# Optimization experiments

Measured on AMD Instinct MI355X. Metric: run time of the kernel, lower is better.

## Reference

```python
import jax, jax.numpy as jnp
import numpy as np

C = 64            # in_channels
IC = C // 2       # inter_channels (channel_rate=2)
R = 16            # reduction_ratio
EPS = 1e-5


def setup_inputs() -> dict:
    key = jax.random.key(0)
    ks = jax.random.split(key, 16)
    s = 0.05
    return {
        "x": jax.random.normal(ks[0], (16, C, 64, 25), dtype=jnp.float32),
        # 1x1 conv projections (common_v, key, query): [out, in] + bias
        "Wv": jax.random.normal(ks[1], (IC, C), dtype=jnp.float32) * s,
        "bv": jax.random.normal(ks[2], (IC,), dtype=jnp.float32) * s,
        "Wk": jax.random.normal(ks[3], (IC, C), dtype=jnp.float32) * s,
        "bk": jax.random.normal(ks[4], (IC,), dtype=jnp.float32) * s,
        "Wq": jax.random.normal(ks[5], (IC, C), dtype=jnp.float32) * s,
        "bq": jax.random.normal(ks[6], (IC,), dtype=jnp.float32) * s,
        # Trans_s: conv1x1 back to C + BatchNorm2d params (nonzero so output is non-trivial)
        "Wt": jax.random.normal(ks[7], (C, IC), dtype=jnp.float32) * s,
        "bt": jax.random.normal(ks[8], (C,), dtype=jnp.float32) * s,
        "gamma": jax.random.normal(ks[9], (C,), dtype=jnp.float32) * 0.5 + 1.0,
        "beta": jax.random.normal(ks[10], (C,), dtype=jnp.float32) * s,
        # ChannelGate MLP: Linear(C, C//R), Linear(C//R, C)
        "W1": jax.random.normal(ks[11], (C // R, C), dtype=jnp.float32) * s,
        "b1": jax.random.normal(ks[12], (C // R,), dtype=jnp.float32) * s,
        "W2": jax.random.normal(ks[13], (C, C // R), dtype=jnp.float32) * s,
        "b2": jax.random.normal(ks[14], (C,), dtype=jnp.float32) * s,
    }


def _conv1x1(x, W, b):
    # x: [N, Cin, T, V]; W: [Cout, Cin]
    return jnp.einsum('nctv,oc->notv', x, W) + b[None, :, None, None]


def reference(x, Wv, bv, Wk, bk, Wq, bq, Wt, bt, gamma, beta, W1, b1, W2, b2):
    N, Cc, T, V = x.shape
    TV = T * V
    ic = Wv.shape[0]

    v_x = _conv1x1(x, Wv, bv).reshape(N, ic, TV).transpose(0, 2, 1)  # [N, TV, ic]
    k_x = _conv1x1(x, Wk, bk).reshape(N, ic, TV).transpose(0, 2, 1)  # [N, TV, ic]
    q_x = _conv1x1(x, Wq, bq).reshape(N, ic, TV)                      # [N, ic, TV]

    # Unscaled dot-product attention over TV tokens (full [N, TV, TV] matrix)
    A = jnp.einsum('nti,nis->nts', k_x, q_x)
    attn = jax.nn.softmax(A, axis=-1)
    p = jnp.einsum('nts,nsi->nti', attn, v_x)                         # [N, TV, ic]
    p = p.transpose(0, 2, 1).reshape(N, ic, T, V)

    # Trans_s: conv1x1 + BatchNorm2d (training-mode batch statistics)
    p = _conv1x1(p, Wt, bt)
    mean = p.mean(axis=(0, 2, 3), keepdims=True)
    var = p.var(axis=(0, 2, 3), keepdims=True)
    p = (p - mean) * jax.lax.rsqrt(var + EPS)
    p = p * gamma[None, :, None, None] + beta[None, :, None, None]

    # ChannelGate (avg pool only) applied to original x
    avg = x.mean(axis=(2, 3))                                          # [N, C]
    h = jax.nn.relu(avg @ W1.T + b1)
    gate = jax.nn.sigmoid(h @ W2.T + b2)                               # [N, C]

    return gate[:, :, None, None] * p + x
```

## Files before the change

### kernel.cpp

```cpp
#include <hip/hip_runtime.h>
#include <hip/hip_bf16.h>
#include <math.h>

#define NB   16
#define CC   64
#define ICH  32
#define TV   1600
#define NTV  (NB*TV)

typedef __bf16 bf16x8 __attribute__((ext_vector_type(8)));
typedef __bf16 bf16x4 __attribute__((ext_vector_type(4)));
typedef float  f32x4  __attribute__((ext_vector_type(4)));

__global__ __launch_bounds__(256) void proj_gate_kernel(
    const float* __restrict__ x,
    const float* __restrict__ Wv, const float* __restrict__ bv,
    const float* __restrict__ Wk, const float* __restrict__ bk,
    const float* __restrict__ Wq, const float* __restrict__ bq,
    __bf16* __restrict__ Qb, __bf16* __restrict__ Kb,
    __bf16* __restrict__ VTb, float* __restrict__ AVG) {
  if (blockIdx.x >= 1248) {
    int b = blockIdx.x - 1248;
    int n = b >> 2, cq = b & 3;
    int c16 = threadIdx.x >> 4, l = threadIdx.x & 15;
    int c = cq * 16 + c16;
    const float4* xp = (const float4*)(x + ((size_t)n * CC + c) * TV) + l;
    float s = 0.f;
#pragma unroll
    for (int i = 0; i < 25; ++i) {
      float4 v = xp[i * 16];
      s += v.x + v.y + v.z + v.w;
    }
#pragma unroll
    for (int off = 8; off >= 1; off >>= 1) s += __shfl_down(s, off, 16);
    if (l == 0) AVG[n * CC + c] = s * (1.0f / (float)TV);
    return;
  }

  int r = blockIdx.x & 7;
  int i = blockIdx.x >> 3;
  int g = i / 12, sub = i % 12;
  int tile = r + 8 * g;
  if (tile >= 100) return;

  int p = sub >> 2, og = sub & 3;
  int ob = og * 8;
  int tvIdx = tile * 256 + threadIdx.x;
  int n = tvIdx / TV, tv = tvIdx % TV;

  const float* W; const float* B;
  if (p == 0)      { W = Wv; B = bv; }
  else if (p == 1) { W = Wk; B = bk; }
  else             { W = Wq; B = bq; }

  float acc[8];
#pragma unroll
  for (int j = 0; j < 8; ++j) acc[j] = B[ob + j];

  const float* xp = x + (size_t)n * CC * TV + tv;
#pragma unroll 16
  for (int c = 0; c < CC; ++c) {
    float xc = xp[c * TV];
#pragma unroll
    for (int j = 0; j < 8; ++j)
      acc[j] = fmaf(W[(ob + j) * CC + c], xc, acc[j]);
  }

  if (p == 0) {
#pragma unroll
    for (int j = 0; j < 8; ++j)
      VTb[(n * ICH + ob + j) * TV + tv] = (__bf16)acc[j];
  } else {
    if (p == 1) {
#pragma unroll
      for (int j = 0; j < 8; ++j)
        acc[j] *= 1.4426950408889634f;
    }
    bf16x8 t;
#pragma unroll
    for (int j = 0; j < 8; ++j) t[j] = (__bf16)acc[j];
    int base = (n * TV + tv) * ICH + ob;
    if (p == 1) *(bf16x8*)(Qb + base) = t;
    else        *(bf16x8*)(Kb + base) = t;
  }
}

__global__ __launch_bounds__(256) void attn_kernel(
    const __bf16* __restrict__ Qb, const __bf16* __restrict__ Kb,
    const __bf16* __restrict__ VTb, __bf16* __restrict__ P,
    const float* __restrict__ Wt, const float* __restrict__ bt,
    float* __restrict__ GSP) {
  __shared__ float smem_f[7936];
  int b = blockIdx.x;
  int r8 = b & 7, qq = b >> 3;
  int n = r8 * 2 + (qq >= 50 ? 1 : 0);
  int rowTile = (qq >= 50) ? qq - 50 : qq;
  int row0 = rowTile * 32;

  int w = threadIdx.x >> 6;
  int lane = threadIdx.x & 63;
  int m = lane & 15, q = lane >> 4;

  __bf16* Pw = (__bf16*)smem_f + w * 2304;

  const __bf16* Qn = Qb  + (size_t)n * TV * ICH;
  const __bf16* Kn = Kb  + (size_t)n * TV * ICH;
  const __bf16* Vn = VTb + (size_t)n * ICH * TV;

  bf16x8 aQ0 = *(const bf16x8*)(Qn + (row0 + m) * ICH + q * 8);
  bf16x8 aQ1 = *(const bf16x8*)(Qn + (row0 + 16 + m) * ICH + q * 8);

  f32x4 o00 = {0.f,0.f,0.f,0.f}, o01 = {0.f,0.f,0.f,0.f};
  f32x4 o10 = {0.f,0.f,0.f,0.f}, o11 = {0.f,0.f,0.f,0.f};
  float ls0 = 0.f, ls1 = 0.f;
  const f32x4 zero = {0.f,0.f,0.f,0.f};

  int ow = (w + b) & 3;
  int nch = (ow == 0) ? 7 : 6;

  bf16x8 bKc[4], pVc[2][2];
  {
    int s0 = ow * 64;
#pragma unroll
    for (int st = 0; st < 4; ++st)
      bKc[st] = *(const bf16x8*)(Kn + (s0 + st * 16 + m) * ICH + q * 8);
#pragma unroll
    for (int kc = 0; kc < 2; ++kc)
#pragma unroll
      for (int ict = 0; ict < 2; ++ict)
        pVc[kc][ict] = *(const bf16x8*)(Vn + (ict * 16 + m) * TV + s0 + kc * 32 + q * 8);
  }

  for (int j = 0; j < nch; ++j) {
#pragma unroll
    for (int st = 0; st < 4; ++st) {
      __builtin_amdgcn_s_setprio(1);
      f32x4 a0 = __builtin_amdgcn_mfma_f32_16x16x32_bf16(bKc[st], aQ0, zero, 0, 0, 0);
      f32x4 a1 = __builtin_amdgcn_mfma_f32_16x16x32_bf16(bKc[st], aQ1, zero, 0, 0, 0);
      __builtin_amdgcn_s_setprio(0);
      bf16x4 t0, t1;
#pragma unroll
      for (int r = 0; r < 4; ++r) {
        float e0 = __builtin_amdgcn_exp2f(a0[r]); ls0 += e0; t0[r] = (__bf16)e0;
        float e1 = __builtin_amdgcn_exp2f(a1[r]); ls1 += e1; t1[r] = (__bf16)e1;
      }
      int off = m * 72 + st * 16 + q * 4;
      *(bf16x4*)(Pw + off)        = t0;
      *(bf16x4*)(Pw + 1152 + off) = t1;
    }
    int chn = 4 * (j + 1) + ow;
    int s0n = (chn < 25 ? chn : 0) * 64;
    bf16x8 bKn[4], pVn[2][2];
#pragma unroll
    for (int st = 0; st < 4; ++st)
      bKn[st] = *(const bf16x8*)(Kn + (s0n + st * 16 + m) * ICH + q * 8);
#pragma unroll
    for (int kc = 0; kc < 2; ++kc)
#pragma unroll
      for (int ict = 0; ict < 2; ++ict)
        pVn[kc][ict] = *(const bf16x8*)(Vn + (ict * 16 + m) * TV + s0n + kc * 32 + q * 8);
    asm volatile("s_waitcnt lgkmcnt(0)" ::: "memory");
#pragma unroll
    for (int kc = 0; kc < 2; ++kc) {
      bf16x8 aP0 = *(const bf16x8*)(Pw + m * 72 + kc * 32 + q * 8);
      bf16x8 aP1 = *(const bf16x8*)(Pw + 1152 + m * 72 + kc * 32 + q * 8);
      __builtin_amdgcn_s_setprio(1);
      o00 = __builtin_amdgcn_mfma_f32_16x16x32_bf16(aP0, pVc[kc][0], o00, 0, 0, 0);
      o10 = __builtin_amdgcn_mfma_f32_16x16x32_bf16(aP1, pVc[kc][0], o10, 0, 0, 0);
      o01 = __builtin_amdgcn_mfma_f32_16x16x32_bf16(aP0, pVc[kc][1], o01, 0, 0, 0);
      o11 = __builtin_amdgcn_mfma_f32_16x16x32_bf16(aP1, pVc[kc][1], o11, 0, 0, 0);
      __builtin_amdgcn_s_setprio(0);
    }
#pragma unroll
    for (int st = 0; st < 4; ++st) bKc[st] = bKn[st];
#pragma unroll
    for (int kc = 0; kc < 2; ++kc)
#pragma unroll
      for (int ict = 0; ict < 2; ++ict) pVc[kc][ict] = pVn[kc][ict];
  }

  ls0 += __shfl_xor(ls0, 16, 64); ls0 += __shfl_xor(ls0, 32, 64);
  ls1 += __shfl_xor(ls1, 16, 64); ls1 += __shfl_xor(ls1, 32, 64);
  f32x4 lv0, lv1;
#pragma unroll
  for (int r = 0; r < 4; ++r) {
    int src = q * 4 + r;
    lv0[r] = __shfl(ls0, src, 64);
    lv1[r] = __shfl(ls1, src, 64);
  }

  float* pub = smem_f;
  float* Pl  = smem_f + 6144;
  float* red = smem_f + 7296;

  __syncthreads();
  f32x4* mp = (f32x4*)(pub + (w * 64 + lane) * 24);
  mp[0] = o00; mp[1] = o01; mp[2] = o10; mp[3] = o11;
  mp[4] = lv0; mp[5] = lv1;
  __syncthreads();

  {
    int lsIdx = 4 + (w >> 1);
    const f32x4* p0 = (const f32x4*)(pub + lane * 24);
    f32x4 osum = p0[w];
    f32x4 lsum = p0[lsIdx];
#pragma unroll
    for (int ww = 1; ww < 4; ++ww) {
      const f32x4* pp = (const f32x4*)(pub + (ww * 64 + lane) * 24);
      f32x4 ov = pp[w], lv = pp[lsIdx];
#pragma unroll
      for (int r = 0; r < 4; ++r) { osum[r] += ov[r]; lsum[r] += lv[r]; }
    }
    int tile = w >> 1, colh = (w & 1) * 16;
#pragma unroll
    for (int r = 0; r < 4; ++r) {
      float p = osum[r] / lsum[r];
      int row = tile * 16 + q * 4 + r;
      P[(n * TV + row0 + row) * ICH + colh + m] = (__bf16)p;
      Pl[row * 36 + colh + m] = p;
    }
  }
  __syncthreads();

  int c = threadIdx.x & 63;
  float wr[ICH];
#pragma unroll
  for (int i = 0; i < ICH; ++i) wr[i] = Wt[c * ICH + i];
  float bc = bt[c];
  float sy = 0.f, sy2 = 0.f;
#pragma unroll
  for (int rr = 0; rr < 8; ++rr) {
    const f32x4* pr = (const f32x4*)(Pl + (w * 8 + rr) * 36);
    float y = bc;
#pragma unroll
    for (int u = 0; u < 8; ++u) {
      f32x4 pv = pr[u];
#pragma unroll
      for (int k = 0; k < 4; ++k) y = fmaf(wr[u * 4 + k], pv[k], y);
    }
    sy += y; sy2 += y * y;
  }
  red[w * 128 + c]      = sy;
  red[w * 128 + 64 + c] = sy2;
  __syncthreads();
  if (threadIdx.x < 128) {
    int t = threadIdx.x;
    float s = red[t] + red[128 + t] + red[256 + t] + red[384 + t];
    GSP[(size_t)t * 800 + b] = s;
  }
}

__global__ __launch_bounds__(256) void apply_kernel(
    const __bf16* __restrict__ P, const float* __restrict__ Wt,
    const float* __restrict__ bt, const float* __restrict__ GSP,
    const float* __restrict__ gamma, const float* __restrict__ beta,
    const float* __restrict__ AVG,
    const float* __restrict__ W1, const float* __restrict__ b1,
    const float* __restrict__ W2, const float* __restrict__ b2,
    const float* __restrict__ x, float* __restrict__ out) {
  int r = blockIdx.x & 7;
  int i = blockIdx.x >> 3;
  int cg = i & 7, h = i >> 3;
  int tb = r + 8 * h;
  if (tb >= 100) return;

  int tvIdx = tb * 256 + threadIdx.x;
  int n = tvIdx / TV, tv = tvIdx % TV;

  __shared__ float sstat[16];
  __shared__ float sSS[16];
  __shared__ float sG[8];

  {
    int colid = threadIdx.x >> 4;
    int sub = threadIdx.x & 15;
    int c8 = colid & 7;
    int gc = (colid < 8) ? (cg * 8 + c8) : (64 + cg * 8 + c8);
    const float* gp = GSP + (size_t)gc * 800;
    float s = 0.f;
#pragma unroll
    for (int k = 0; k < 50; ++k) s += gp[sub + k * 16];
#pragma unroll
    for (int off = 8; off >= 1; off >>= 1) s += __shfl_down(s, off, 16);
    if (sub == 0) sstat[colid] = s;
  }
  __syncthreads();
  if (threadIdx.x < 8) {
    int c8 = threadIdx.x;
    int c = cg * 8 + c8;
    float mean = sstat[c8] * (1.f / (float)NTV);
    float var  = sstat[8 + c8] * (1.f / (float)NTV) - mean * mean;
    float scale = rsqrtf(var + 1e-5f) * gamma[c];
    sSS[c8] = scale;
    sSS[8 + c8] = beta[c] - mean * scale;
    float hh[4];
#pragma unroll
    for (int jj = 0; jj < 4; ++jj) {
      float hv = b1[jj];
      for (int c2 = 0; c2 < CC; ++c2)
        hv = fmaf(W1[jj * CC + c2], AVG[n * CC + c2], hv);
      hh[jj] = fmaxf(hv, 0.f);
    }
    float g = b2[c];
#pragma unroll
    for (int jj = 0; jj < 4; ++jj) g = fmaf(W2[c * 4 + jj], hh[jj], g);
    sG[c8] = 1.f / (1.f + __expf(-g));
  }
  __syncthreads();

  float f[ICH];
  const bf16x8* pp = (const bf16x8*)(P + ((size_t)(n * TV + tv)) * ICH);
#pragma unroll
  for (int u = 0; u < 4; ++u) {
    bf16x8 v = pp[u];
#pragma unroll
    for (int j = 0; j < 8; ++j) f[u * 8 + j] = (float)v[j];
  }

#pragma unroll
  for (int j = 0; j < 8; ++j) {
    int c = cg * 8 + j;
    float y = bt[c];
#pragma unroll
    for (int ii = 0; ii < ICH; ++ii) y = fmaf(Wt[c * ICH + ii], f[ii], y);
    size_t idx = ((size_t)(n * CC + c)) * TV + tv;
    out[idx] = sG[j] * fmaf(y, sSS[j], sSS[8 + j]) + x[idx];
  }
}

extern "C" void kernel_launch(void* const* d_in, const int* in_sizes, int n_in,
                              void* d_out, int out_size, void* d_ws, size_t ws_size,
                              hipStream_t stream) {
  const float* x     = (const float*)d_in[0];
  const float* Wv    = (const float*)d_in[1];
  const float* bv    = (const float*)d_in[2];
  const float* Wk    = (const float*)d_in[3];
  const float* bk    = (const float*)d_in[4];
  const float* Wq    = (const float*)d_in[5];
  const float* bq    = (const float*)d_in[6];
  const float* Wt    = (const float*)d_in[7];
  const float* bt    = (const float*)d_in[8];
  const float* gamma = (const float*)d_in[9];
  const float* beta  = (const float*)d_in[10];
  const float* W1    = (const float*)d_in[11];
  const float* b1    = (const float*)d_in[12];
  const float* W2    = (const float*)d_in[13];
  const float* b2    = (const float*)d_in[14];
  float* out = (float*)d_out;
  char* ws = (char*)d_ws;

  const size_t E = 819200;
  __bf16* Qb  = (__bf16*)(ws);
  __bf16* Kb  = (__bf16*)(ws + 2*E);
  __bf16* VTb = (__bf16*)(ws + 4*E);
  __bf16* Pb  = (__bf16*)(ws + 6*E);
  float*  GSP = (float*) (ws + 8*E);
  float*  AVG = (float*) (ws + 8*E + 409600);

  proj_gate_kernel<<<1312, 256, 0, stream>>>(x, Wv, bv, Wk, bk, Wq, bq,
                                             Qb, Kb, VTb, AVG);
  attn_kernel<<<NB * 50, 256, 0, stream>>>(Qb, Kb, VTb, Pb, Wt, bt, GSP);
  apply_kernel<<<832, 256, 0, stream>>>(Pb, Wt, bt, GSP, gamma, beta, AVG,
                                        W1, b1, W2, b2, x, out);
}
```

Baseline: 138.7 us.

## Software-pipeline attention loop with double-buffered P tiles across chunks

```diff
diff --git a/kernel.cpp b/kernel.cpp
--- a/kernel.cpp
+++ b/kernel.cpp
@@ -90,7 +90,7 @@
     const __bf16* __restrict__ VTb, __bf16* __restrict__ P,
     const float* __restrict__ Wt, const float* __restrict__ bt,
     float* __restrict__ GSP) {
-  __shared__ float smem_f[7936];
+  __shared__ float smem_f[9216];
   int b = blockIdx.x;
   int r8 = b & 7, qq = b >> 3;
   int n = r8 * 2 + (qq >= 50 ? 1 : 0);
@@ -101,7 +101,8 @@
   int lane = threadIdx.x & 63;
   int m = lane & 15, q = lane >> 4;
 
-  __bf16* Pw = (__bf16*)smem_f + w * 2304;
+  __bf16* Pw0 = (__bf16*)smem_f + w * 4608;
+  __bf16* Pw1 = Pw0 + 2304;
 
   const __bf16* Qn = Qb  + (size_t)n * TV * ICH;
   const __bf16* Kn = Kb  + (size_t)n * TV * ICH;
@@ -119,25 +120,16 @@
   int nch = (ow == 0) ? 7 : 6;
 
   bf16x8 bKc[4], pVc[2][2];
+
   {
     int s0 = ow * 64;
 #pragma unroll
     for (int st = 0; st < 4; ++st)
       bKc[st] = *(const bf16x8*)(Kn + (s0 + st * 16 + m) * ICH + q * 8);
 #pragma unroll
-    for (int kc = 0; kc < 2; ++kc)
-#pragma unroll
-      for (int ict = 0; ict < 2; ++ict)
-        pVc[kc][ict] = *(const bf16x8*)(Vn + (ict * 16 + m) * TV + s0 + kc * 32 + q * 8);
-  }
-
-  for (int j = 0; j < nch; ++j) {
-#pragma unroll
     for (int st = 0; st < 4; ++st) {
-      __builtin_amdgcn_s_setprio(1);
       f32x4 a0 = __builtin_amdgcn_mfma_f32_16x16x32_bf16(bKc[st], aQ0, zero, 0, 0, 0);
       f32x4 a1 = __builtin_amdgcn_mfma_f32_16x16x32_bf16(bKc[st], aQ1, zero, 0, 0, 0);
-      __builtin_amdgcn_s_setprio(0);
       bf16x4 t0, t1;
 #pragma unroll
       for (int r = 0; r < 4; ++r) {
@@ -145,38 +137,68 @@
         float e1 = __builtin_amdgcn_exp2f(a1[r]); ls1 += e1; t1[r] = (__bf16)e1;
       }
       int off = m * 72 + st * 16 + q * 4;
-      *(bf16x4*)(Pw + off)        = t0;
-      *(bf16x4*)(Pw + 1152 + off) = t1;
-    }
-    int chn = 4 * (j + 1) + ow;
-    int s0n = (chn < 25 ? chn : 0) * 64;
-    bf16x8 bKn[4], pVn[2][2];
+      *(bf16x4*)(Pw0 + off)        = t0;
+      *(bf16x4*)(Pw0 + 1152 + off) = t1;
+    }
+    int c1 = (4 + ow) * 64;
 #pragma unroll
     for (int st = 0; st < 4; ++st)
-      bKn[st] = *(const bf16x8*)(Kn + (s0n + st * 16 + m) * ICH + q * 8);
+      bKc[st] = *(const bf16x8*)(Kn + (c1 + st * 16 + m) * ICH + q * 8);
 #pragma unroll
     for (int kc = 0; kc < 2; ++kc)
 #pragma unroll
       for (int ict = 0; ict < 2; ++ict)
-        pVn[kc][ict] = *(const bf16x8*)(Vn + (ict * 16 + m) * TV + s0n + kc * 32 + q * 8);
+        pVc[kc][ict] = *(const bf16x8*)(Vn + (ict * 16 + m) * TV + s0 + kc * 32 + q * 8);
+  }
+
+  for (int j = 0; j < nch; ++j) {
+    __bf16* rbuf = (j & 1) ? Pw1 : Pw0;
+    __bf16* wbuf = (j & 1) ? Pw0 : Pw1;
     asm volatile("s_waitcnt lgkmcnt(0)" ::: "memory");
-#pragma unroll
-    for (int kc = 0; kc < 2; ++kc) {
-      bf16x8 aP0 = *(const bf16x8*)(Pw + m * 72 + kc * 32 + q * 8);
-      bf16x8 aP1 = *(const bf16x8*)(Pw + 1152 + m * 72 + kc * 32 + q * 8);
-      __builtin_amdgcn_s_setprio(1);
-      o00 = __builtin_amdgcn_mfma_f32_16x16x32_bf16(aP0, pVc[kc][0], o00, 0, 0, 0);
-      o10 = __builtin_amdgcn_mfma_f32_16x16x32_bf16(aP1, pVc[kc][0], o10, 0, 0, 0);
-      o01 = __builtin_amdgcn_mfma_f32_16x16x32_bf16(aP0, pVc[kc][1], o01, 0, 0, 0);
-      o11 = __builtin_amdgcn_mfma_f32_16x16x32_bf16(aP1, pVc[kc][1], o11, 0, 0, 0);
-      __builtin_amdgcn_s_setprio(0);
-    }
-#pragma unroll
-    for (int st = 0; st < 4; ++st) bKc[st] = bKn[st];
-#pragma unroll
-    for (int kc = 0; kc < 2; ++kc)
-#pragma unroll
-      for (int ict = 0; ict < 2; ++ict) pVc[kc][ict] = pVn[kc][ict];
+    bf16x8 aP00 = *(const bf16x8*)(rbuf + m * 72 +      q * 8);
+    bf16x8 aP01 = *(const bf16x8*)(rbuf + m * 72 + 32 + q * 8);
+    bf16x8 aP10 = *(const bf16x8*)(rbuf + 1152 + m * 72 +      q * 8);
+    bf16x8 aP11 = *(const bf16x8*)(rbuf + 1152 + m * 72 + 32 + q * 8);
+    if (j + 1 < nch) {
+#pragma unroll
+      for (int st = 0; st < 4; ++st) {
+        f32x4 a0 = __builtin_amdgcn_mfma_f32_16x16x32_bf16(bKc[st], aQ0, zero, 0, 0, 0);
+        f32x4 a1 = __builtin_amdgcn_mfma_f32_16x16x32_bf16(bKc[st], aQ1, zero, 0, 0, 0);
+        bf16x4 t0, t1;
+#pragma unroll
+        for (int r = 0; r < 4; ++r) {
+          float e0 = __builtin_amdgcn_exp2f(a0[r]); ls0 += e0; t0[r] = (__bf16)e0;
+          float e1 = __builtin_amdgcn_exp2f(a1[r]); ls1 += e1; t1[r] = (__bf16)e1;
+        }
+        int off = m * 72 + st * 16 + q * 4;
+        *(bf16x4*)(wbuf + off)        = t0;
+        *(bf16x4*)(wbuf + 1152 + off) = t1;
+      }
+    }
+    {
+      int chn = 4 * (j + 2) + ow;
+      int s0n = (chn < 25 ? chn : 0) * 64;
+#pragma unroll
+      for (int st = 0; st < 4; ++st)
+        bKc[st] = *(const bf16x8*)(Kn + (s0n + st * 16 + m) * ICH + q * 8);
+    }
+    o00 = __builtin_amdgcn_mfma_f32_16x16x32_bf16(aP00, pVc[0][0], o00, 0, 0, 0);
+    o10 = __builtin_amdgcn_mfma_f32_16x16x32_bf16(aP10, pVc[0][0], o10, 0, 0, 0);
+    o01 = __builtin_amdgcn_mfma_f32_16x16x32_bf16(aP00, pVc[0][1], o01, 0, 0, 0);
+    o11 = __builtin_amdgcn_mfma_f32_16x16x32_bf16(aP10, pVc[0][1], o11, 0, 0, 0);
+    o00 = __builtin_amdgcn_mfma_f32_16x16x32_bf16(aP01, pVc[1][0], o00, 0, 0, 0);
+    o10 = __builtin_amdgcn_mfma_f32_16x16x32_bf16(aP11, pVc[1][0], o10, 0, 0, 0);
+    o01 = __builtin_amdgcn_mfma_f32_16x16x32_bf16(aP01, pVc[1][1], o01, 0, 0, 0);
+    o11 = __builtin_amdgcn_mfma_f32_16x16x32_bf16(aP11, pVc[1][1], o11, 0, 0, 0);
+    {
+      int chv = 4 * (j + 1) + ow;
+      int s0v = (chv < 25 ? chv : 0) * 64;
+#pragma unroll
+      for (int kc = 0; kc < 2; ++kc)
+#pragma unroll
+        for (int ict = 0; ict < 2; ++ict)
+          pVc[kc][ict] = *(const bf16x8*)(Vn + (ict * 16 + m) * TV + s0v + kc * 32 + q * 8);
+    }
   }
 
   ls0 += __shfl_xor(ls0, 16, 64); ls0 += __shfl_xor(ls0, 32, 64);
```

New measurement: 136.8 us. About the same (-1.4%).
